# Kernel optimization log

Measured on AMD Instinct MI355X. Metric: run time of the kernel, lower is better.

The kernel has to match this reference:

```python
import jax, jax.numpy as jnp
import numpy as np

DIM = 320; HEADS = 8; DHEAD = 40; CTX_DIM = 768
INNER = HEADS * DHEAD; FF_INNER = 4 * DIM
B = 1; N = 4096; M = 77
SCALE = DHEAD ** -0.5


def setup_inputs() -> dict:
    key = jax.random.key(0)
    ks = jax.random.split(key, 16)
    p = lambda i, shape: jax.random.normal(ks[i], shape, dtype=jnp.float32) * 0.02
    return {
        "x": jax.random.normal(ks[0], (B, N, DIM), dtype=jnp.float32),
        "context": jax.random.normal(ks[1], (B, M, CTX_DIM), dtype=jnp.float32),
        "focused_attention_mask": jax.random.uniform(ks[2], (1, M, M), dtype=jnp.float32),
        "g1": jnp.ones((DIM,), jnp.float32), "b1": jnp.zeros((DIM,), jnp.float32),
        "g2": jnp.ones((DIM,), jnp.float32), "b2": jnp.zeros((DIM,), jnp.float32),
        "g3": jnp.ones((DIM,), jnp.float32), "b3": jnp.zeros((DIM,), jnp.float32),
        "Wq1": p(3, (DIM, INNER)), "Wk1": p(4, (DIM, INNER)), "Wv1": p(5, (DIM, INNER)),
        "Wo1": p(6, (INNER, DIM)), "bo1": jnp.zeros((DIM,), jnp.float32),
        "Wq2": p(7, (DIM, INNER)), "Wk2": p(8, (CTX_DIM, INNER)), "Wv2": p(9, (CTX_DIM, INNER)),
        "Wo2": p(10, (INNER, DIM)), "bo2": jnp.zeros((DIM,), jnp.float32),
        "Wff1": p(11, (DIM, 2 * FF_INNER)), "bff1": jnp.zeros((2 * FF_INNER,), jnp.float32),
        "Wff2": p(12, (FF_INNER, DIM)), "bff2": jnp.zeros((DIM,), jnp.float32),
        "use_fca": 1,
    }


def _ln(x, g, b):
    mu = x.mean(-1, keepdims=True)
    var = jnp.mean((x - mu) ** 2, -1, keepdims=True)
    return (x - mu) * jax.lax.rsqrt(var + 1e-5) * g + b


def _attn(xn, ctx, Wq, Wk, Wv, Wo, bo, fam, use_fca):
    b, n, _ = xn.shape
    heads = lambda t: t.reshape(b, t.shape[1], HEADS, DHEAD).transpose(0, 2, 1, 3)  # b h n d
    q, k, v = heads(xn @ Wq), heads(ctx @ Wk), heads(ctx @ Wv)
    sim = jnp.einsum('bhid,bhjd->bhij', q, k) * SCALE
    if use_fca:
        m = fam.shape[-1]  # fam: [1, m, m], batch must be 1 (repeat_interleave semantics)
        fw = jnp.einsum('bhqk,dk->bhqd', sim[..., :m], fam[0])
        fw = jnp.minimum(jnp.abs(fw), 1.0)
        fw = fw / (jnp.max(fw, axis=-1, keepdims=True) + 1e-6)
        fw = (fw > 0.6).astype(sim.dtype)
        sim = sim.at[..., :m].add((fw - 1.0) * 50.0)
    a = jax.nn.softmax(sim, axis=-1)
    o = jnp.einsum('bhij,bhjd->bhid', a, v).transpose(0, 2, 1, 3).reshape(b, n, INNER)
    return o @ Wo + bo


def reference(x, context, focused_attention_mask,
              g1, b1, g2, b2, g3, b3,
              Wq1, Wk1, Wv1, Wo1, bo1,
              Wq2, Wk2, Wv2, Wo2, bo2,
              Wff1, bff1, Wff2, bff2, use_fca):
    # attn1: self-attention (context=None in original -> use_fca forced to 0)
    h1 = _ln(x, g1, b1)
    x = _attn(h1, h1, Wq1, Wk1, Wv1, Wo1, bo1, None, 0) + x
    # attn2: cross-attention with focused-attention mask
    h2 = _ln(x, g2, b2)
    x = _attn(h2, context, Wq2, Wk2, Wv2, Wo2, bo2, focused_attention_mask, int(use_fca)) + x
    # GEGLU feed-forward
    h3 = _ln(x, g3, b3)
    proj = h3 @ Wff1 + bff1
    a_, gate = jnp.split(proj, 2, axis=-1)
    x = (a_ * jax.nn.gelu(gate, approximate=False)) @ Wff2 + bff2 + x
    return x
```

## Files before the change

kernel.cpp:

```cpp
#include <hip/hip_runtime.h>
#include <math.h>

typedef __bf16 bf16_t;
typedef __bf16 bf16x8 __attribute__((ext_vector_type(8)));
typedef __bf16 bf16x4 __attribute__((ext_vector_type(4)));
typedef float  f32x4  __attribute__((ext_vector_type(4)));
typedef _Float16 f16_t;
typedef _Float16 f16x4 __attribute__((ext_vector_type(4)));
typedef _Float16 f16x8 __attribute__((ext_vector_type(8)));
typedef __fp16 hf16x2 __attribute__((ext_vector_type(2)));

static constexpr float ATT_SCALE = 0.15811388300841897f;
static constexpr float SC2 = 0.22811031f;
static constexpr float LOG2E = 1.4426950408889634f;

__device__ __forceinline__ bf16_t f2b(float f) {
  unsigned u = __float_as_uint(f);
  u = (u + 0x7fffu + ((u >> 16) & 1u)) >> 16;
  unsigned short s = (unsigned short)u;
  bf16_t r;
  *(unsigned short*)&r = s;
  return r;
}
__device__ __forceinline__ float b2f(bf16_t b) {
  unsigned short s = *(const unsigned short*)&b;
  return __uint_as_float(((unsigned)s) << 16);
}
__device__ __forceinline__ void sto(float v, float* p)  { *p = v; }
__device__ __forceinline__ void sto(float v, bf16_t* p) { *p = f2b(v); }
__device__ __forceinline__ unsigned pkh2(float a, float b) {
  hf16x2 h = __builtin_amdgcn_cvt_pkrtz(a, b);
  return *(unsigned*)&h;
}

__global__ __launch_bounds__(256) void prep_ln_kernel(
    const float* __restrict__ Wq1, const float* __restrict__ Wk1, const float* __restrict__ Wv1,
    const float* __restrict__ Wo1, const float* __restrict__ Wq2,
    const float* __restrict__ Wk2, const float* __restrict__ Wv2, const float* __restrict__ Wo2,
    const float* __restrict__ Wff1, const float* __restrict__ Wff2,
    const float* __restrict__ fam,
    bf16_t* __restrict__ wqkvt, bf16_t* __restrict__ wo1t, float* __restrict__ wkv2t,
    bf16_t* __restrict__ wo2t, bf16_t* __restrict__ wff1t, bf16_t* __restrict__ wff2t,
    bf16_t* __restrict__ wq2th, bf16_t* __restrict__ wq2tl,
    bf16_t* __restrict__ famh, bf16_t* __restrict__ faml,
    bf16_t* __restrict__ zpad,
    const float* __restrict__ x, const float* __restrict__ g1, const float* __restrict__ b1,
    bf16_t* __restrict__ h1b)
{
  const int b = blockIdx.x;
  const int tid = threadIdx.x;

  if (b >= 634) {
    const int bb = b - 634;
    const int lane = tid & 63;
    const int row = bb * 4 + (tid >> 6);
    const float* xr = x + (size_t)row * 320;
    float v[5], s = 0.f, s2 = 0.f;
#pragma unroll
    for (int i = 0; i < 5; i++) { v[i] = xr[lane + i*64]; s += v[i]; s2 += v[i]*v[i]; }
#pragma unroll
    for (int o = 32; o; o >>= 1) { s += __shfl_xor(s, o); s2 += __shfl_xor(s2, o); }
    float mu = s * (1.f/320.f);
    float rs = rsqrtf(fmaxf(s2*(1.f/320.f) - mu*mu, 0.f) + 1e-5f);
#pragma unroll
    for (int i = 0; i < 5; i++) {
      int c = lane + i*64;
      h1b[(size_t)row*320 + c] = f2b((v[i]-mu)*rs*g1[c] + b1[c]);
    }
    return;
  }

  if (b >= 570) {
    for (int idx = (b - 570)*256 + tid; idx < 9216 + 135168; idx += 64*256) {
      if (idx < 9216) {
        int d = idx / 96, k = idx - d*96;
        float v = (d < 77 && k < 77) ? fam[d*77 + k] : 0.f;
        bf16_t h = f2b(v);
        famh[idx] = h;
        faml[idx] = f2b(v - b2f(h));
      } else {
        zpad[idx - 9216] = f2b(0.f);
      }
    }
    return;
  }

  __shared__ float T[64][65];
  const float* src; int S, O, n0, k0, mode;
  float scale = 1.f;
  bf16_t* outb = nullptr; float* outf = nullptr;
  int nadj;

  if (b < 75) {
    int tn = b / 5, tk = b - tn*5;
    n0 = tn*64; k0 = tk*64; S = 320; O = 320; mode = 0; outb = wqkvt;
    if (n0 < 320)      { src = Wq1; nadj = n0;       scale = SC2; }
    else if (n0 < 640) { src = Wk1; nadj = n0 - 320; }
    else               { src = Wv1; nadj = n0 - 640; }
  } else if (b < 100) {
    int b2 = b - 75; int tn = b2 / 5, tk = b2 - tn*5;
    n0 = tn*64; k0 = tk*64; S = 320; O = 320; mode = 0; outb = wo1t; src = Wo1; nadj = n0;
  } else if (b < 220) {
    int b2 = b - 100; int tn = b2 / 12, tk = b2 - tn*12;
    n0 = tn*64; k0 = tk*64; S = 320; O = 768; mode = 1; outf = wkv2t;
    if (n0 < 320) { src = Wk2; nadj = n0; } else { src = Wv2; nadj = n0 - 320; }
  } else if (b < 245) {
    int b2 = b - 220; int tn = b2 / 5, tk = b2 - tn*5;
    n0 = tn*64; k0 = tk*64; S = 320; O = 320; mode = 0; outb = wo2t; src = Wo2; nadj = n0;
  } else if (b < 445) {
    int b2 = b - 245; int tn = b2 / 5, tk = b2 - tn*5;
    n0 = tn*64; k0 = tk*64; S = 2560; O = 320; mode = 0; outb = wff1t; src = Wff1; nadj = n0;
  } else if (b < 545) {
    int b2 = b - 445; int tn = b2 / 20, tk = b2 - tn*20;
    n0 = tn*64; k0 = tk*64; S = 320; O = 1280; mode = 0; outb = wff2t; src = Wff2; nadj = n0;
  } else {
    int b2 = b - 545; int tn = b2 / 5, tk = b2 - tn*5;
    n0 = tn*64; k0 = tk*64; S = 320; O = 320; mode = 2; src = Wq2; nadj = n0;
  }

  const int r4 = tid >> 6;
  const int c  = tid & 63;
  const float* srcp = src + nadj;
#pragma unroll
  for (int i = 0; i < 16; i++) {
    int r = i*4 + r4;
    T[c][r] = srcp[(size_t)(k0 + r)*S + c] * scale;
  }
  __syncthreads();
#pragma unroll
  for (int i = 0; i < 16; i++) {
    int r = i*4 + r4;
    float v = T[r][c];
    size_t oi = (size_t)(n0 + r)*O + k0 + c;
    if (mode == 0) {
      outb[oi] = f2b(v);
    } else if (mode == 1) {
      outf[oi] = v;
    } else {
      bf16_t h = f2b(v);
      wq2th[oi] = h;
      wq2tl[oi] = f2b(v - b2f(h));
    }
  }
}

template<typename OT>
__global__ __launch_bounds__(256) void ln_kernel(
    const float* __restrict__ x, const float* __restrict__ g, const float* __restrict__ b,
    OT* __restrict__ out)
{
  const int lane = threadIdx.x & 63;
  const int row = blockIdx.x * 4 + (threadIdx.x >> 6);
  const float* xr = x + (size_t)row * 320;
  float v[5], s = 0.f, s2 = 0.f;
#pragma unroll
  for (int i = 0; i < 5; i++) { v[i] = xr[lane + i*64]; s += v[i]; s2 += v[i]*v[i]; }
#pragma unroll
  for (int o = 32; o; o >>= 1) { s += __shfl_xor(s, o); s2 += __shfl_xor(s2, o); }
  float mu = s * (1.f/320.f);
  float rs = rsqrtf(fmaxf(s2*(1.f/320.f) - mu*mu, 0.f) + 1e-5f);
#pragma unroll
  for (int i = 0; i < 5; i++) {
    int c = lane + i*64;
    sto((v[i]-mu)*rs*g[c] + b[c], &out[(size_t)row*320 + c]);
  }
}

__global__ __launch_bounds__(256) void ln2_split_kernel(
    const float* __restrict__ x, const float* __restrict__ g, const float* __restrict__ b,
    bf16_t* __restrict__ hi, bf16_t* __restrict__ lo)
{
  const int lane = threadIdx.x & 63;
  const int row = blockIdx.x * 4 + (threadIdx.x >> 6);
  const float* xr = x + (size_t)row * 320;
  float v[5], s = 0.f, s2 = 0.f;
#pragma unroll
  for (int i = 0; i < 5; i++) { v[i] = xr[lane + i*64]; s += v[i]; s2 += v[i]*v[i]; }
#pragma unroll
  for (int o = 32; o; o >>= 1) { s += __shfl_xor(s, o); s2 += __shfl_xor(s2, o); }
  float mu = s * (1.f/320.f);
  float rs = rsqrtf(fmaxf(s2*(1.f/320.f) - mu*mu, 0.f) + 1e-5f);
#pragma unroll
  for (int i = 0; i < 5; i++) {
    int c = lane + i*64;
    float y = (v[i]-mu)*rs*g[c] + b[c];
    bf16_t h = f2b(y);
    hi[(size_t)row*320 + c] = h;
    lo[(size_t)row*320 + c] = f2b(y - b2f(h));
  }
}

__global__ __launch_bounds__(256) void kv2_dot_kernel(
    const float* __restrict__ ctx, const float* __restrict__ wkv2t,
    bf16_t* __restrict__ k2h, bf16_t* __restrict__ k2l, bf16_t* __restrict__ v2t)
{
  __shared__ float4 Bs[16][193];
  const int tid = threadIdx.x;
  const int nb = blockIdx.x % 40, ms = blockIdx.x / 40;
  const int n0 = nb*16;
  for (int e = tid; e < 16*192; e += 256) {
    int row = e / 192, c4 = e - row*192;
    Bs[row][c4] = *(const float4*)(wkv2t + (size_t)(n0+row)*768 + c4*4);
  }
  __syncthreads();
  const int g = tid >> 4, q = tid & 15;
  const int mlo = ms*20;
  const int mhi = (mlo + 20 > 77) ? 77 : mlo + 20;
  for (int m = mlo; m < mhi; m++) {
    const float4* a = (const float4*)(ctx + (size_t)m*768);
    float acc = 0.f;
#pragma unroll
    for (int i = 0; i < 12; i++) {
      float4 av = a[i*16+q], bv = Bs[g][i*16+q];
      acc += av.x*bv.x + av.y*bv.y + av.z*bv.z + av.w*bv.w;
    }
#pragma unroll
    for (int o = 8; o; o >>= 1) acc += __shfl_xor(acc, o);
    if (q == 0) {
      int n = n0 + g;
      if (n < 320) {
        int h = n / 40, d = n - h*40;
        int idx = h*6144 + m*64 + d;
        bf16_t hh = f2b(acc);
        k2h[idx] = hh;
        k2l[idx] = f2b(acc - b2f(hh));
      } else {
        int n2 = n - 320; int h = n2 / 40, d = n2 - h*40;
        v2t[h*4608 + d*96 + m] = f2b(acc);
      }
    }
  }
}

__global__ __launch_bounds__(256) void repack_vt_kernel(
    const bf16_t* __restrict__ qkvb, f16_t* __restrict__ vpack, bf16_t* __restrict__ kpack)
{
  __shared__ f16_t T[64*44];
  const int tid = threadIdx.x;
  const int t0 = blockIdx.x * 64, h = blockIdx.y;
  for (int e = tid; e < 320; e += 256) {
    int t = e / 5, c8 = (e - t*5) * 8;
    bf16x8 v = *(const bf16x8*)(qkvb + (size_t)(t0+t)*960 + 640 + h*40 + c8);
    f16_t* dst = &T[t*44 + c8];
#pragma unroll
    for (int j = 0; j < 8; j++) dst[j] = (f16_t)b2f(v[j]);
  }
  __syncthreads();
  for (int e = tid; e < 3072; e += 256) {
    int dt = e >> 10;
    int r  = e & 1023;
    int g2 = r >> 9, o = r & 511;
    int lane = o >> 3, j = o & 7;
    int qd = lane >> 4, ln = lane & 15;
    int d = dt*16 + ln;
    int key = g2*32 + ((j & 4) ? 16 : 0) + qd*4 + (j & 3);
    float val;
    if (d < 40)       val = (float)T[key*44 + d];
    else if (d == 40) val = 1.0f;
    else              val = 0.0f;
    vpack[(((size_t)h*3 + dt)*128 + (t0 >> 5) + g2)*512 + o] = (f16_t)val;
  }
  for (int e = tid; e < 2560; e += 256) {
    int g = e / 640, o = e - g*640;
    int key = t0 + g*16;
    bf16_t val;
    if (o < 512) {
      int lane = o >> 3, j = o & 7;
      int qd = lane >> 4, ln = lane & 15;
      val = qkvb[(size_t)(key + ln)*960 + 320 + h*40 + qd*8 + j];
    } else {
      int o2 = o - 512; int ln = o2 >> 3, j = o2 & 7;
      val = qkvb[(size_t)(key + ln)*960 + 320 + h*40 + 32 + j];
    }
    kpack[((size_t)h*256 + (t0 >> 4) + g)*640 + o] = val;
  }
}

__global__ __launch_bounds__(512, 4) void flash_self_kernel(
    const bf16_t* __restrict__ qkvb, const bf16_t* __restrict__ kpack,
    const f16_t* __restrict__ vpack,
    bf16_t* __restrict__ o1a)
{
  __shared__ float Red[12288];
  const int tid = threadIdx.x;
  const int w = tid >> 6, lane = tid & 63;
  const int ln = lane & 15, qd = lane >> 4;
  const int qh = w >> 2, kh = w & 3;
  const int h = blockIdx.x & 7;
  const int q0 = (blockIdx.x >> 3) * 64;

  const int kgbase = h*256 + kh*2;
  const int vgbase = h*384 + kh;
  const int lko = lane*8;

  bf16x8 zero8 = {};
  bf16x8 bq[2][2];
#pragma unroll
  for (int nt = 0; nt < 2; nt++) {
    const bf16_t* qp = qkvb + (size_t)(q0 + qh*32 + nt*16 + ln)*960 + h*40;
    bq[nt][0] = *(const bf16x8*)(qp + qd*8);
    bq[nt][1] = (qd == 0) ? *(const bf16x8*)(qp + 32) : zero8;
  }

  f32x4 zero4 = {0.f,0.f,0.f,0.f};
  f32x4 oacc[3][2];
#pragma unroll
  for (int a = 0; a < 3; a++)
#pragma unroll
    for (int b = 0; b < 2; b++) oacc[a][b] = zero4;

#define FS_LOADK(DST, K0)                                                       \
  {                                                                             \
    const bf16_t* kp_ = kpack + ((size_t)kgbase + ((K0) >> 4)) * 640;           \
    DST[0][0] = *(const bf16x8*)(kp_ + lko);                                    \
    DST[0][1] = (qd == 0) ? *(const bf16x8*)(kp_ + 512 + ln*8) : zero8;         \
    DST[1][0] = *(const bf16x8*)(kp_ + 640 + lko);                              \
    DST[1][1] = (qd == 0) ? *(const bf16x8*)(kp_ + 1152 + ln*8) : zero8;        \
  }

#define FS_LOADV(DST, K0)                                                       \
  {                                                                             \
    _Pragma("unroll")                                                           \
    for (int dt_ = 0; dt_ < 3; dt_++)                                           \
      DST[dt_] = *(const f16x8*)(vpack + ((size_t)vgbase + dt_*128 + ((K0) >> 5)) * 512 + lko); \
  }

#define FS_COMPUTE(KA, VA)                                                      \
  {                                                                             \
    __builtin_amdgcn_s_setprio(1);                                              \
    _Pragma("unroll")                                                           \
    for (int nt = 0; nt < 2; nt++) {                                            \
      f32x4 s0 = __builtin_amdgcn_mfma_f32_16x16x32_bf16(KA[0][0], bq[nt][0], zero4, 0,0,0); \
      s0 = __builtin_amdgcn_mfma_f32_16x16x32_bf16(KA[0][1], bq[nt][1], s0, 0,0,0); \
      f32x4 s1 = __builtin_amdgcn_mfma_f32_16x16x32_bf16(KA[1][0], bq[nt][0], zero4, 0,0,0); \
      s1 = __builtin_amdgcn_mfma_f32_16x16x32_bf16(KA[1][1], bq[nt][1], s1, 0,0,0); \
      uint4 u_;                                                                 \
      u_.x = pkh2(__builtin_amdgcn_exp2f(s0[0]), __builtin_amdgcn_exp2f(s0[1])); \
      u_.y = pkh2(__builtin_amdgcn_exp2f(s0[2]), __builtin_amdgcn_exp2f(s0[3])); \
      u_.z = pkh2(__builtin_amdgcn_exp2f(s1[0]), __builtin_amdgcn_exp2f(s1[1])); \
      u_.w = pkh2(__builtin_amdgcn_exp2f(s1[2]), __builtin_amdgcn_exp2f(s1[3])); \
      f16x8 pb = *(f16x8*)&u_;                                                  \
      _Pragma("unroll")                                                         \
      for (int dt = 0; dt < 3; dt++)                                            \
        oacc[dt][nt] = __builtin_amdgcn_mfma_f32_16x16x32_f16(VA[dt], pb, oacc[dt][nt], 0,0,0); \
    }                                                                           \
    __builtin_amdgcn_s_setprio(0);                                              \
  }

  bf16x8 ka[2][2], kb[2][2];
  f16x8 va[3], vb[3];
  FS_LOADK(ka, 0);
  FS_LOADV(va, 0);
#pragma unroll 1
  for (int it = 0; it < 32; it += 2) {
    const int k0 = it*128;
    FS_LOADK(kb, k0 + 128);
    FS_LOADV(vb, k0 + 128);
    FS_COMPUTE(ka, va);
    FS_LOADK(ka, (it + 2 < 32) ? (k0 + 256) : 0);
    FS_LOADV(va, (it + 2 < 32) ? (k0 + 256) : 0);
    FS_COMPUTE(kb, vb);
  }
#undef FS_LOADK
#undef FS_LOADV
#undef FS_COMPUTE

#pragma unroll
  for (int nt = 0; nt < 2; nt++)
#pragma unroll
    for (int dt = 0; dt < 3; dt++)
      *(f32x4*)&Red[((w*2 + nt)*3 + dt)*256 + ln*16 + qd*4] = oacc[dt][nt];
  __syncthreads();
  const int dgrp = tid & 7, lq = (tid >> 3) & 15, ntw = (tid >> 7) & 1, qh2 = tid >> 8;
  float l = Red[(((qh2*4 + 0)*2 + ntw)*3 + 2)*256 + lq*16 + 8]
          + Red[(((qh2*4 + 1)*2 + ntw)*3 + 2)*256 + lq*16 + 8]
          + Red[(((qh2*4 + 2)*2 + ntw)*3 + 2)*256 + lq*16 + 8]
          + Red[(((qh2*4 + 3)*2 + ntw)*3 + 2)*256 + lq*16 + 8];
  float inv = 1.f / l;
  bf16_t* obase = o1a + (size_t)(q0 + qh2*32 + ntw*16 + lq)*320 + h*40;
#pragma unroll
  for (int i = 0; i < 5; i++) {
    int d = dgrp + i*8;
    int dt = d >> 4, dr = d & 15;
    float o = Red[(((qh2*4 + 0)*2 + ntw)*3 + dt)*256 + lq*16 + dr]
            + Red[(((qh2*4 + 1)*2 + ntw)*3 + dt)*256 + lq*16 + dr]
            + Red[(((qh2*4 + 2)*2 + ntw)*3 + dt)*256 + lq*16 + dr]
            + Red[(((qh2*4 + 3)*2 + ntw)*3 + dt)*256 + lq*16 + dr];
    obase[d] = f2b(o * inv);
  }
}

__global__ __launch_bounds__(256) void attn_cross_kernel(
    const float* __restrict__ q2, const bf16_t* __restrict__ k2h, const bf16_t* __restrict__ k2l,
    const bf16_t* __restrict__ famh, const bf16_t* __restrict__ faml,
    const bf16_t* __restrict__ v2t, const int* __restrict__ use_fca,
    bf16_t* __restrict__ o2)
{
  __shared__ bf16_t SMh[4][16*96];
  __shared__ bf16_t SMl[4][16*96];
  __shared__ bf16_t PAs[4][16*96];
  const int tid = threadIdx.x;
  const int w = tid >> 6, lane = tid & 63;
  const int ln = lane & 15, qd = lane >> 4;
  const int h = blockIdx.x & 7;
  const int q0 = (blockIdx.x >> 3)*64 + w*16;
  const int fca = use_fca[0];
  bf16_t* smh = SMh[w];
  bf16_t* sml = SMl[w];
  bf16_t* pa  = PAs[w];

  {
    bf16x4 z = {};
    int q = lane >> 2, c = 80 + (lane & 3)*4;
    *(bf16x4*)&smh[q*96 + c] = z;
    *(bf16x4*)&sml[q*96 + c] = z;
    *(bf16x4*)&pa [q*96 + c] = z;
  }

  bf16x8 zero8 = {};
  bf16x8 aqh0, aql0, aqh1 = zero8, aql1 = zero8;
  {
    const float* qp = q2 + (size_t)(q0 + ln)*320 + h*40;
    float4 v0 = *(const float4*)(qp + qd*8);
    float4 v1 = *(const float4*)(qp + qd*8 + 4);
    float qv[8] = {v0.x,v0.y,v0.z,v0.w,v1.x,v1.y,v1.z,v1.w};
#pragma unroll
    for (int i = 0; i < 8; i++) {
      bf16_t hh = f2b(qv[i]);
      aqh0[i] = hh; aql0[i] = f2b(qv[i] - b2f(hh));
    }
    if (qd == 0) {
      float4 u0 = *(const float4*)(qp + 32);
      float4 u1 = *(const float4*)(qp + 36);
      float uv[8] = {u0.x,u0.y,u0.z,u0.w,u1.x,u1.y,u1.z,u1.w};
#pragma unroll
      for (int i = 0; i < 8; i++) {
        bf16_t hh = f2b(uv[i]);
        aqh1[i] = hh; aql1[i] = f2b(uv[i] - b2f(hh));
      }
    }
  }

  f32x4 zero4 = {0.f,0.f,0.f,0.f};
  float ss[5][4];
  __builtin_amdgcn_s_setprio(1);
#pragma unroll
  for (int nt = 0; nt < 5; nt++) {
    const bf16_t* kb = k2h + ((size_t)h*96 + nt*16 + ln)*64 + qd*8;
    const bf16_t* kl = k2l + ((size_t)h*96 + nt*16 + ln)*64 + qd*8;
    bf16x8 kh0 = *(const bf16x8*)kb;
    bf16x8 kh1 = *(const bf16x8*)(kb + 32);
    bf16x8 kl0 = *(const bf16x8*)kl;
    bf16x8 kl1 = *(const bf16x8*)(kl + 32);
    f32x4 s;
    s = __builtin_amdgcn_mfma_f32_16x16x32_bf16(aqh0, kl0, zero4, 0, 0, 0);
    s = __builtin_amdgcn_mfma_f32_16x16x32_bf16(aql0, kh0, s, 0, 0, 0);
    s = __builtin_amdgcn_mfma_f32_16x16x32_bf16(aqh0, kh0, s, 0, 0, 0);
    s = __builtin_amdgcn_mfma_f32_16x16x32_bf16(aqh1, kl1, s, 0, 0, 0);
    s = __builtin_amdgcn_mfma_f32_16x16x32_bf16(aql1, kh1, s, 0, 0, 0);
    s = __builtin_amdgcn_mfma_f32_16x16x32_bf16(aqh1, kh1, s, 0, 0, 0);
#pragma unroll
    for (int r = 0; r < 4; r++) {
      float sv = s[r] * ATT_SCALE;
      ss[nt][r] = sv;
      bf16_t hh = f2b(sv);
      smh[(qd*4 + r)*96 + nt*16 + ln] = hh;
      sml[(qd*4 + r)*96 + nt*16 + ln] = f2b(sv - b2f(hh));
    }
  }
  __builtin_amdgcn_s_setprio(0);

  f32x4 facc[5];
#pragma unroll
  for (int nt = 0; nt < 5; nt++) facc[nt] = zero4;
  __builtin_amdgcn_s_setprio(1);
#pragma unroll
  for (int c = 0; c < 3; c++) {
    bf16x8 sah = *(const bf16x8*)&smh[ln*96 + c*32 + qd*8];
    bf16x8 sal = *(const bf16x8*)&sml[ln*96 + c*32 + qd*8];
#pragma unroll
    for (int nt = 0; nt < 5; nt++) {
      bf16x8 fh8 = *(const bf16x8*)(famh + ((size_t)(nt*16 + ln))*96 + c*32 + qd*8);
      bf16x8 fl8 = *(const bf16x8*)(faml + ((size_t)(nt*16 + ln))*96 + c*32 + qd*8);
      facc[nt] = __builtin_amdgcn_mfma_f32_16x16x32_bf16(sah, fl8, facc[nt], 0, 0, 0);
      facc[nt] = __builtin_amdgcn_mfma_f32_16x16x32_bf16(sal, fh8, facc[nt], 0, 0, 0);
      facc[nt] = __builtin_amdgcn_mfma_f32_16x16x32_bf16(sah, fh8, facc[nt], 0, 0, 0);
    }
  }
  __builtin_amdgcn_s_setprio(0);

  float pr[5][4];
  if (fca) {
    float fwv[5][4], fm[4];
#pragma unroll
    for (int nt = 0; nt < 5; nt++)
#pragma unroll
      for (int r = 0; r < 4; r++) fwv[nt][r] = fminf(fabsf(facc[nt][r]), 1.f);
#pragma unroll
    for (int r = 0; r < 4; r++) {
      float m = fmaxf(fmaxf(fwv[0][r], fwv[1][r]), fmaxf(fwv[2][r], fmaxf(fwv[3][r], fwv[4][r])));
#pragma unroll
      for (int o = 8; o; o >>= 1) m = fmaxf(m, __shfl_xor(m, o));
      fm[r] = m;
    }
#pragma unroll
    for (int nt = 0; nt < 5; nt++)
#pragma unroll
      for (int r = 0; r < 4; r++) {
        float lg = ss[nt][r] - ((fwv[nt][r] > 0.6f*(fm[r] + 1e-6f)) ? 0.f : 50.f);
        pr[nt][r] = __builtin_amdgcn_exp2f(lg * LOG2E);
      }
  } else {
#pragma unroll
    for (int nt = 0; nt < 5; nt++)
#pragma unroll
      for (int r = 0; r < 4; r++)
        pr[nt][r] = __builtin_amdgcn_exp2f(ss[nt][r] * LOG2E);
  }
  if (ln >= 13) {
#pragma unroll
    for (int r = 0; r < 4; r++) pr[4][r] = 0.f;
  }
  float l_[4] = {0.f,0.f,0.f,0.f};
#pragma unroll
  for (int nt = 0; nt < 5; nt++)
#pragma unroll
    for (int r = 0; r < 4; r++) {
      l_[r] += pr[nt][r];
      pa[(qd*4 + r)*96 + nt*16 + ln] = f2b(pr[nt][r]);
    }
#pragma unroll
  for (int r = 0; r < 4; r++)
#pragma unroll
    for (int o = 8; o; o >>= 1) l_[r] += __shfl_xor(l_[r], o);

  f32x4 oacc[3];
#pragma unroll
  for (int nt = 0; nt < 3; nt++) oacc[nt] = zero4;
  __builtin_amdgcn_s_setprio(1);
#pragma unroll
  for (int c = 0; c < 3; c++) {
    bf16x8 paf = *(const bf16x8*)&pa[ln*96 + c*32 + qd*8];
#pragma unroll
    for (int nt = 0; nt < 3; nt++) {
      bf16x8 vb = *(const bf16x8*)(v2t + ((size_t)h*48 + nt*16 + ln)*96 + c*32 + qd*8);
      oacc[nt] = __builtin_amdgcn_mfma_f32_16x16x32_bf16(paf, vb, oacc[nt], 0, 0, 0);
    }
  }
  __builtin_amdgcn_s_setprio(0);
  float inv[4];
#pragma unroll
  for (int r = 0; r < 4; r++) inv[r] = 1.f / l_[r];
#pragma unroll
  for (int nt = 0; nt < 3; nt++) {
    int d = nt*16 + ln;
    if (d < 40) {
#pragma unroll
      for (int r = 0; r < 4; r++)
        o2[(size_t)(q0 + qd*4 + r)*320 + h*40 + d] = f2b(oacc[nt][r]*inv[r]);
    }
  }
}

template<int OUT_BF16>
__global__ __launch_bounds__(256) void gemm_bf16_kernel(
    const bf16_t* __restrict__ A, const bf16_t* __restrict__ Bt,
    const float* __restrict__ bias, const float* __restrict__ resid,
    void* __restrict__ Cout, int M, int N, int K)
{
  __shared__ bf16_t As[128][72];
  __shared__ bf16_t Bs[64][72];
  const int tid = threadIdx.x;
  const int m0 = blockIdx.x * 128, n0 = blockIdx.y * 64;
  const int w = tid >> 6, lane = tid & 63;
  const int wr = w >> 1, wc = w & 1;
  const int ln = lane & 15, qd = lane >> 4;
  f32x4 zero = {0.f, 0.f, 0.f, 0.f};
  f32x4 acc[4][2];
#pragma unroll
  for (int a = 0; a < 4; a++)
#pragma unroll
    for (int b = 0; b < 2; b++) acc[a][b] = zero;

  for (int k0 = 0; k0 < K; k0 += 64) {
    __syncthreads();
#pragma unroll
    for (int i = 0; i < 4; i++) {
      int vid = tid + i*256;
      int r = vid >> 3, c8 = (vid & 7) * 8;
      *(bf16x8*)&As[r][c8] = *(const bf16x8*)(A + (size_t)(m0+r)*K + k0 + c8);
    }
#pragma unroll
    for (int i = 0; i < 2; i++) {
      int vid = tid + i*256;
      int r = vid >> 3, c8 = (vid & 7) * 8;
      *(bf16x8*)&Bs[r][c8] = *(const bf16x8*)(Bt + (size_t)(n0+r)*K + k0 + c8);
    }
    __syncthreads();
#pragma unroll
    for (int c = 0; c < 2; c++) {
      bf16x8 af[4], bfr[2];
#pragma unroll
      for (int mt = 0; mt < 4; mt++)
        af[mt] = *(const bf16x8*)&As[wr*64 + mt*16 + ln][c*32 + qd*8];
#pragma unroll
      for (int nt = 0; nt < 2; nt++)
        bfr[nt] = *(const bf16x8*)&Bs[wc*32 + nt*16 + ln][c*32 + qd*8];
#pragma unroll
      for (int mt = 0; mt < 4; mt++)
#pragma unroll
        for (int nt = 0; nt < 2; nt++)
          acc[mt][nt] = __builtin_amdgcn_mfma_f32_16x16x32_bf16(af[mt], bfr[nt], acc[mt][nt], 0, 0, 0);
    }
  }
#pragma unroll
  for (int mt = 0; mt < 4; mt++)
#pragma unroll
    for (int nt = 0; nt < 2; nt++)
#pragma unroll
      for (int r = 0; r < 4; r++) {
        int gm = m0 + wr*64 + mt*16 + qd*4 + r;
        int gn = n0 + wc*32 + nt*16 + ln;
        float v = acc[mt][nt][r];
        if (bias)  v += bias[gn];
        if (resid) v += resid[(size_t)gm*N + gn];
        if (OUT_BF16) sto(v, &((bf16_t*)Cout)[(size_t)gm*N + gn]);
        else          sto(v, &((float*)Cout)[(size_t)gm*N + gn]);
      }
}

template<int OUT_BF16>
__global__ __launch_bounds__(256) void gemm_bf16_32_kernel(
    const bf16_t* __restrict__ A, const bf16_t* __restrict__ Bt,
    const float* __restrict__ bias, const float* __restrict__ resid,
    void* __restrict__ Cout, int M, int N, int K)
{
  __shared__ bf16_t As[32][72];
  __shared__ bf16_t Bs[64][72];
  const int tid = threadIdx.x;
  const int m0 = blockIdx.x * 32, n0 = blockIdx.y * 64;
  const int w = tid >> 6, lane = tid & 63;
  const int wr = w >> 1, wc = w & 1;
  const int ln = lane & 15, qd = lane >> 4;
  f32x4 zero = {0.f, 0.f, 0.f, 0.f};
  f32x4 acc[2];
  acc[0] = zero; acc[1] = zero;

  for (int k0 = 0; k0 < K; k0 += 64) {
    __syncthreads();
    {
      int r = tid >> 3, c8 = (tid & 7) * 8;
      *(bf16x8*)&As[r][c8] = *(const bf16x8*)(A + (size_t)(m0+r)*K + k0 + c8);
    }
#pragma unroll
    for (int i = 0; i < 2; i++) {
      int vid = tid + i*256;
      int r = vid >> 3, c8 = (vid & 7) * 8;
      *(bf16x8*)&Bs[r][c8] = *(const bf16x8*)(Bt + (size_t)(n0+r)*K + k0 + c8);
    }
    __syncthreads();
#pragma unroll
    for (int c = 0; c < 2; c++) {
      bf16x8 af = *(const bf16x8*)&As[wr*16 + ln][c*32 + qd*8];
#pragma unroll
      for (int nt = 0; nt < 2; nt++) {
        bf16x8 bfr = *(const bf16x8*)&Bs[wc*32 + nt*16 + ln][c*32 + qd*8];
        acc[nt] = __builtin_amdgcn_mfma_f32_16x16x32_bf16(af, bfr, acc[nt], 0, 0, 0);
      }
    }
  }
#pragma unroll
  for (int nt = 0; nt < 2; nt++)
#pragma unroll
    for (int r = 0; r < 4; r++) {
      int gm = m0 + wr*16 + qd*4 + r;
      int gn = n0 + wc*32 + nt*16 + ln;
      float v = acc[nt][r];
      if (bias)  v += bias[gn];
      if (resid) v += resid[(size_t)gm*N + gn];
      if (OUT_BF16) sto(v, &((bf16_t*)Cout)[(size_t)gm*N + gn]);
      else          sto(v, &((float*)Cout)[(size_t)gm*N + gn]);
    }
}

__global__ __launch_bounds__(256) void gemm3_32_kernel(
    const bf16_t* __restrict__ Ah, const bf16_t* __restrict__ Al,
    const bf16_t* __restrict__ Bth, const bf16_t* __restrict__ Btl,
    float* __restrict__ C, int M, int N, int K)
{
  __shared__ bf16_t Ash[32][72];
  __shared__ bf16_t Asl[32][72];
  __shared__ bf16_t Bsh[64][72];
  __shared__ bf16_t Bsl[64][72];
  const int tid = threadIdx.x;
  const int m0 = blockIdx.x * 32, n0 = blockIdx.y * 64;
  const int w = tid >> 6, lane = tid & 63;
  const int wr = w >> 1, wc = w & 1;
  const int ln = lane & 15, qd = lane >> 4;
  f32x4 zero = {0.f, 0.f, 0.f, 0.f};
  f32x4 acc[2];
  acc[0] = zero; acc[1] = zero;

  for (int k0 = 0; k0 < K; k0 += 64) {
    __syncthreads();
    {
      int r = tid >> 3, c8 = (tid & 7) * 8;
      *(bf16x8*)&Ash[r][c8] = *(const bf16x8*)(Ah + (size_t)(m0+r)*K + k0 + c8);
      *(bf16x8*)&Asl[r][c8] = *(const bf16x8*)(Al + (size_t)(m0+r)*K + k0 + c8);
    }
#pragma unroll
    for (int i = 0; i < 2; i++) {
      int vid = tid + i*256;
      int r = vid >> 3, c8 = (vid & 7) * 8;
      *(bf16x8*)&Bsh[r][c8] = *(const bf16x8*)(Bth + (size_t)(n0+r)*K + k0 + c8);
      *(bf16x8*)&Bsl[r][c8] = *(const bf16x8*)(Btl + (size_t)(n0+r)*K + k0 + c8);
    }
    __syncthreads();
#pragma unroll
    for (int c = 0; c < 2; c++) {
      bf16x8 afh = *(const bf16x8*)&Ash[wr*16 + ln][c*32 + qd*8];
      bf16x8 afl = *(const bf16x8*)&Asl[wr*16 + ln][c*32 + qd*8];
#pragma unroll
      for (int nt = 0; nt < 2; nt++) {
        bf16x8 bfh = *(const bf16x8*)&Bsh[wc*32 + nt*16 + ln][c*32 + qd*8];
        bf16x8 bfl = *(const bf16x8*)&Bsl[wc*32 + nt*16 + ln][c*32 + qd*8];
        acc[nt] = __builtin_amdgcn_mfma_f32_16x16x32_bf16(afh, bfl, acc[nt], 0, 0, 0);
        acc[nt] = __builtin_amdgcn_mfma_f32_16x16x32_bf16(afl, bfh, acc[nt], 0, 0, 0);
        acc[nt] = __builtin_amdgcn_mfma_f32_16x16x32_bf16(afh, bfh, acc[nt], 0, 0, 0);
      }
    }
  }
#pragma unroll
  for (int nt = 0; nt < 2; nt++)
#pragma unroll
    for (int r = 0; r < 4; r++) {
      int gm = m0 + wr*16 + qd*4 + r;
      int gn = n0 + wc*32 + nt*16 + ln;
      C[(size_t)gm*N + gn] = acc[nt][r];
    }
}

__global__ __launch_bounds__(256) void gemm_geglu_kernel(
    const bf16_t* __restrict__ A, const bf16_t* __restrict__ Bt,
    const float* __restrict__ bias, bf16_t* __restrict__ gg, int K)
{
  __shared__ bf16_t As[128][72];
  __shared__ bf16_t Ba[64][72];
  __shared__ bf16_t Bg[64][72];
  const int tid = threadIdx.x;
  const int m0 = blockIdx.x * 128, n0 = blockIdx.y * 64;
  const int w = tid >> 6, lane = tid & 63;
  const int wr = w >> 1, wc = w & 1;
  const int ln = lane & 15, qd = lane >> 4;
  f32x4 zero = {0.f, 0.f, 0.f, 0.f};
  f32x4 acca[4][2], accg[4][2];
#pragma unroll
  for (int a = 0; a < 4; a++)
#pragma unroll
    for (int b = 0; b < 2; b++) { acca[a][b] = zero; accg[a][b] = zero; }

  for (int k0 = 0; k0 < K; k0 += 64) {
    __syncthreads();
#pragma unroll
    for (int i = 0; i < 4; i++) {
      int vid = tid + i*256;
      int r = vid >> 3, c8 = (vid & 7) * 8;
      *(bf16x8*)&As[r][c8] = *(const bf16x8*)(A + (size_t)(m0+r)*K + k0 + c8);
    }
#pragma unroll
    for (int i = 0; i < 2; i++) {
      int vid = tid + i*256;
      int r = vid >> 3, c8 = (vid & 7) * 8;
      *(bf16x8*)&Ba[r][c8] = *(const bf16x8*)(Bt + (size_t)(n0+r)*K + k0 + c8);
      *(bf16x8*)&Bg[r][c8] = *(const bf16x8*)(Bt + (size_t)(n0+r+1280)*K + k0 + c8);
    }
    __syncthreads();
#pragma unroll
    for (int c = 0; c < 2; c++) {
      bf16x8 af[4], ba[2], bg[2];
#pragma unroll
      for (int mt = 0; mt < 4; mt++)
        af[mt] = *(const bf16x8*)&As[wr*64 + mt*16 + ln][c*32 + qd*8];
#pragma unroll
      for (int nt = 0; nt < 2; nt++) {
        ba[nt] = *(const bf16x8*)&Ba[wc*32 + nt*16 + ln][c*32 + qd*8];
        bg[nt] = *(const bf16x8*)&Bg[wc*32 + nt*16 + ln][c*32 + qd*8];
      }
#pragma unroll
      for (int mt = 0; mt < 4; mt++)
#pragma unroll
        for (int nt = 0; nt < 2; nt++) {
          acca[mt][nt] = __builtin_amdgcn_mfma_f32_16x16x32_bf16(af[mt], ba[nt], acca[mt][nt], 0, 0, 0);
          accg[mt][nt] = __builtin_amdgcn_mfma_f32_16x16x32_bf16(af[mt], bg[nt], accg[mt][nt], 0, 0, 0);
        }
    }
  }
#pragma unroll
  for (int mt = 0; mt < 4; mt++)
#pragma unroll
    for (int nt = 0; nt < 2; nt++)
#pragma unroll
      for (int r = 0; r < 4; r++) {
        int gm = m0 + wr*64 + mt*16 + qd*4 + r;
        int gn = n0 + wc*32 + nt*16 + ln;
        float va = acca[mt][nt][r] + bias[gn];
        float vg = accg[mt][nt][r] + bias[1280 + gn];
        float ge = 0.5f * vg * (1.f + erff(vg * 0.70710678118654752f));
        gg[(size_t)gm*1280 + gn] = f2b(va * ge);
      }
}

extern "C" void kernel_launch(void* const* d_in, const int* in_sizes, int n_in,
                              void* d_out, int out_size, void* d_ws, size_t ws_size,
                              hipStream_t stream)
{
  const float* x    = (const float*)d_in[0];
  const float* ctx  = (const float*)d_in[1];
  const float* fam  = (const float*)d_in[2];
  const float* g1   = (const float*)d_in[3];
  const float* b1   = (const float*)d_in[4];
  const float* g2   = (const float*)d_in[5];
  const float* b2   = (const float*)d_in[6];
  const float* g3   = (const float*)d_in[7];
  const float* b3   = (const float*)d_in[8];
  const float* Wq1  = (const float*)d_in[9];
  const float* Wk1  = (const float*)d_in[10];
  const float* Wv1  = (const float*)d_in[11];
  const float* Wo1  = (const float*)d_in[12];
  const float* bo1  = (const float*)d_in[13];
  const float* Wq2  = (const float*)d_in[14];
  const float* Wk2  = (const float*)d_in[15];
  const float* Wv2  = (const float*)d_in[16];
  const float* Wo2  = (const float*)d_in[17];
  const float* bo2  = (const float*)d_in[18];
  const float* Wff1 = (const float*)d_in[19];
  const float* bff1 = (const float*)d_in[20];
  const float* Wff2 = (const float*)d_in[21];
  const float* bff2 = (const float*)d_in[22];
  const int*   ufca = (const int*)d_in[23];

  char* ws = (char*)d_ws;
  bf16_t* qkvb = (bf16_t*)(ws + 0);
  f16_t*  vpack = (f16_t*)(ws + 7864320);
  bf16_t* kpack = (bf16_t*)(ws + 11010048);
  bf16_t* h1b  = (bf16_t*)(ws + 13631488);
  bf16_t* h2hi = (bf16_t*)(ws + 16252928);
  bf16_t* h2lo = (bf16_t*)(ws + 18874368);
  float*  x2   = (float*)(ws + 21495808);
  float*  q2   = (float*)(ws + 26738688);
  bf16_t* o1a  = (bf16_t*)(ws + 26738688);
  bf16_t* o2   = (bf16_t*)(ws + 32178688);
  float*  x3   = (float*)(ws + 34800128);
  bf16_t* h3b  = (bf16_t*)(ws + 40043008);
  bf16_t* wqkvt = (bf16_t*)(ws + 42664448);
  bf16_t* wo1t  = (bf16_t*)(ws + 43278848);
  float*  wkv2t = (float*)(ws + 43483648);
  bf16_t* wo2t  = (bf16_t*)(ws + 45449728);
  bf16_t* wff1t = (bf16_t*)(ws + 45654528);
  bf16_t* wff2t = (bf16_t*)(ws + 47292928);
  bf16_t* wq2th = (bf16_t*)(ws + 48374272);
  bf16_t* wq2tl = (bf16_t*)(ws + 48579072);
  bf16_t* famh  = (bf16_t*)(ws + 48783872);
  bf16_t* faml  = (bf16_t*)(ws + 48802304);
  bf16_t* k2h   = (bf16_t*)(ws + 48820736);
  bf16_t* k2l   = (bf16_t*)(ws + 48919040);
  bf16_t* v2t   = (bf16_t*)(ws + 49017344);
  bf16_t* gg   = (bf16_t*)(ws + 21495808);

  float* xout = (float*)d_out;

  prep_ln_kernel<<<1658, 256, 0, stream>>>(Wq1, Wk1, Wv1, Wo1, Wq2, Wk2, Wv2, Wo2, Wff1, Wff2, fam,
                                           wqkvt, wo1t, wkv2t, wo2t, wff1t, wff2t, wq2th, wq2tl,
                                           famh, faml, k2h, x, g1, b1, h1b);
  gemm_bf16_kernel<1><<<dim3(32,15), 256, 0, stream>>>(h1b, wqkvt, nullptr, nullptr, qkvb, 4096, 960, 320);
  repack_vt_kernel<<<dim3(64,8), 256, 0, stream>>>(qkvb, vpack, kpack);
  flash_self_kernel<<<512, 512, 0, stream>>>(qkvb, kpack, vpack, o1a);
  gemm_bf16_32_kernel<0><<<dim3(128,5), 256, 0, stream>>>(o1a, wo1t, bo1, x, x2, 4096, 320, 320);
  ln2_split_kernel<<<1024, 256, 0, stream>>>(x2, g2, b2, h2hi, h2lo);
  gemm3_32_kernel<<<dim3(128,5), 256, 0, stream>>>(h2hi, h2lo, wq2th, wq2tl, q2, 4096, 320, 320);
  kv2_dot_kernel<<<160, 256, 0, stream>>>(ctx, wkv2t, k2h, k2l, v2t);
  attn_cross_kernel<<<512, 256, 0, stream>>>(q2, k2h, k2l, famh, faml, v2t, ufca, o2);
  gemm_bf16_32_kernel<0><<<dim3(128,5), 256, 0, stream>>>(o2, wo2t, bo2, x2, x3, 4096, 320, 320);
  ln_kernel<bf16_t><<<1024, 256, 0, stream>>>(x3, g3, b3, h3b);
  gemm_geglu_kernel<<<dim3(32,20), 256, 0, stream>>>(h3b, wff1t, bff1, gg, 320);
  gemm_bf16_32_kernel<0><<<dim3(128,5), 256, 0, stream>>>(gg, wff2t, bff2, x3, xout, 4096, 320, 1280);
}
```

Before: 258.2 us.

## Load GEMM tiles via direct global-to-LDS loads with XOR-swizzled layout

Replaces the register-staged global loads and LDS stores in the three bf16 GEMM kernels with global_load_lds 16-byte direct transfers into unpadded LDS tiles. The tiles are XOR-swizzled on 16-byte chunks, and the fragment reads use the matching swizzle, so bank conflicts are avoided without the previous padding. This cuts VGPR traffic and instruction count in the load phase. It relies on the 16-byte global_load_lds variant being supported on gfx950, and the swizzle indexing has to be exactly right for correctness.

```diff
diff --git a/kernel.cpp b/kernel.cpp
--- a/kernel.cpp
+++ b/kernel.cpp
@@ -31,6 +31,10 @@
 __device__ __forceinline__ unsigned pkh2(float a, float b) {
   hf16x2 h = __builtin_amdgcn_cvt_pkrtz(a, b);
   return *(unsigned*)&h;
+}
+__device__ __forceinline__ void gl_lds16(const void* g, void* l) {
+  __builtin_amdgcn_global_load_lds((const __attribute__((address_space(1))) unsigned*)g,
+                                   (__attribute__((address_space(3))) unsigned*)l, 16, 0, 0);
 }
 
 __global__ __launch_bounds__(256) void prep_ln_kernel(
@@ -568,13 +572,16 @@
     const float* __restrict__ bias, const float* __restrict__ resid,
     void* __restrict__ Cout, int M, int N, int K)
 {
-  __shared__ bf16_t As[128][72];
-  __shared__ bf16_t Bs[64][72];
+  __shared__ __align__(16) bf16_t As[128][64];
+  __shared__ __align__(16) bf16_t Bs[64][64];
   const int tid = threadIdx.x;
   const int m0 = blockIdx.x * 128, n0 = blockIdx.y * 64;
   const int w = tid >> 6, lane = tid & 63;
   const int wr = w >> 1, wc = w & 1;
   const int ln = lane & 15, qd = lane >> 4;
+  const int lr = lane >> 3, lsw = (lane & 7) ^ lr;
+  char* asb = (char*)&As[0][0];
+  char* bsb = (char*)&Bs[0][0];
   f32x4 zero = {0.f, 0.f, 0.f, 0.f};
   f32x4 acc[4][2];
 #pragma unroll
@@ -585,27 +592,22 @@
   for (int k0 = 0; k0 < K; k0 += 64) {
     __syncthreads();
 #pragma unroll
-    for (int i = 0; i < 4; i++) {
-      int vid = tid + i*256;
-      int r = vid >> 3, c8 = (vid & 7) * 8;
-      *(bf16x8*)&As[r][c8] = *(const bf16x8*)(A + (size_t)(m0+r)*K + k0 + c8);
-    }
-#pragma unroll
-    for (int i = 0; i < 2; i++) {
-      int vid = tid + i*256;
-      int r = vid >> 3, c8 = (vid & 7) * 8;
-      *(bf16x8*)&Bs[r][c8] = *(const bf16x8*)(Bt + (size_t)(n0+r)*K + k0 + c8);
-    }
+    for (int i = 0; i < 4; i++)
+      gl_lds16(A + (size_t)(m0 + (i*4 + w)*8 + lr)*K + k0 + lsw*8, asb + (i*4 + w)*1024);
+#pragma unroll
+    for (int i = 0; i < 2; i++)
+      gl_lds16(Bt + (size_t)(n0 + (i*4 + w)*8 + lr)*K + k0 + lsw*8, bsb + (i*4 + w)*1024);
     __syncthreads();
 #pragma unroll
     for (int c = 0; c < 2; c++) {
+      const int sa = (((c*4 + qd) ^ (ln & 7))) * 8;
       bf16x8 af[4], bfr[2];
 #pragma unroll
       for (int mt = 0; mt < 4; mt++)
-        af[mt] = *(const bf16x8*)&As[wr*64 + mt*16 + ln][c*32 + qd*8];
+        af[mt] = *(const bf16x8*)&As[wr*64 + mt*16 + ln][sa];
 #pragma unroll
       for (int nt = 0; nt < 2; nt++)
-        bfr[nt] = *(const bf16x8*)&Bs[wc*32 + nt*16 + ln][c*32 + qd*8];
+        bfr[nt] = *(const bf16x8*)&Bs[wc*32 + nt*16 + ln][sa];
 #pragma unroll
       for (int mt = 0; mt < 4; mt++)
 #pragma unroll
@@ -635,36 +637,34 @@
     const float* __restrict__ bias, const float* __restrict__ resid,
     void* __restrict__ Cout, int M, int N, int K)
 {
-  __shared__ bf16_t As[32][72];
-  __shared__ bf16_t Bs[64][72];
+  __shared__ __align__(16) bf16_t As[32][64];
+  __shared__ __align__(16) bf16_t Bs[64][64];
   const int tid = threadIdx.x;
   const int m0 = blockIdx.x * 32, n0 = blockIdx.y * 64;
   const int w = tid >> 6, lane = tid & 63;
   const int wr = w >> 1, wc = w & 1;
   const int ln = lane & 15, qd = lane >> 4;
+  const int lr = lane >> 3, lsw = (lane & 7) ^ lr;
+  char* asb = (char*)&As[0][0];
+  char* bsb = (char*)&Bs[0][0];
   f32x4 zero = {0.f, 0.f, 0.f, 0.f};
   f32x4 acc[2];
   acc[0] = zero; acc[1] = zero;
 
   for (int k0 = 0; k0 < K; k0 += 64) {
     __syncthreads();
-    {
-      int r = tid >> 3, c8 = (tid & 7) * 8;
-      *(bf16x8*)&As[r][c8] = *(const bf16x8*)(A + (size_t)(m0+r)*K + k0 + c8);
-    }
-#pragma unroll
-    for (int i = 0; i < 2; i++) {
-      int vid = tid + i*256;
-      int r = vid >> 3, c8 = (vid & 7) * 8;
-      *(bf16x8*)&Bs[r][c8] = *(const bf16x8*)(Bt + (size_t)(n0+r)*K + k0 + c8);
-    }
+    gl_lds16(A + (size_t)(m0 + w*8 + lr)*K + k0 + lsw*8, asb + w*1024);
+#pragma unroll
+    for (int i = 0; i < 2; i++)
+      gl_lds16(Bt + (size_t)(n0 + (i*4 + w)*8 + lr)*K + k0 + lsw*8, bsb + (i*4 + w)*1024);
     __syncthreads();
 #pragma unroll
     for (int c = 0; c < 2; c++) {
-      bf16x8 af = *(const bf16x8*)&As[wr*16 + ln][c*32 + qd*8];
+      const int sa = (((c*4 + qd) ^ (ln & 7))) * 8;
+      bf16x8 af = *(const bf16x8*)&As[wr*16 + ln][sa];
 #pragma unroll
       for (int nt = 0; nt < 2; nt++) {
-        bf16x8 bfr = *(const bf16x8*)&Bs[wc*32 + nt*16 + ln][c*32 + qd*8];
+        bf16x8 bfr = *(const bf16x8*)&Bs[wc*32 + nt*16 + ln][sa];
         acc[nt] = __builtin_amdgcn_mfma_f32_16x16x32_bf16(af, bfr, acc[nt], 0, 0, 0);
       }
     }
@@ -744,14 +744,18 @@
     const bf16_t* __restrict__ A, const bf16_t* __restrict__ Bt,
     const float* __restrict__ bias, bf16_t* __restrict__ gg, int K)
 {
-  __shared__ bf16_t As[128][72];
-  __shared__ bf16_t Ba[64][72];
-  __shared__ bf16_t Bg[64][72];
+  __shared__ __align__(16) bf16_t As[128][64];
+  __shared__ __align__(16) bf16_t Ba[64][64];
+  __shared__ __align__(16) bf16_t Bg[64][64];
   const int tid = threadIdx.x;
   const int m0 = blockIdx.x * 128, n0 = blockIdx.y * 64;
   const int w = tid >> 6, lane = tid & 63;
   const int wr = w >> 1, wc = w & 1;
   const int ln = lane & 15, qd = lane >> 4;
+  const int lr = lane >> 3, lsw = (lane & 7) ^ lr;
+  char* asb = (char*)&As[0][0];
+  char* bab = (char*)&Ba[0][0];
+  char* bgb = (char*)&Bg[0][0];
   f32x4 zero = {0.f, 0.f, 0.f, 0.f};
   f32x4 acca[4][2], accg[4][2];
 #pragma unroll
@@ -762,29 +766,25 @@
   for (int k0 = 0; k0 < K; k0 += 64) {
     __syncthreads();
 #pragma unroll
-    for (int i = 0; i < 4; i++) {
-      int vid = tid + i*256;
-      int r = vid >> 3, c8 = (vid & 7) * 8;
-      *(bf16x8*)&As[r][c8] = *(const bf16x8*)(A + (size_t)(m0+r)*K + k0 + c8);
-    }
+    for (int i = 0; i < 4; i++)
+      gl_lds16(A + (size_t)(m0 + (i*4 + w)*8 + lr)*K + k0 + lsw*8, asb + (i*4 + w)*1024);
 #pragma unroll
     for (int i = 0; i < 2; i++) {
-      int vid = tid + i*256;
-      int r = vid >> 3, c8 = (vid & 7) * 8;
-      *(bf16x8*)&Ba[r][c8] = *(const bf16x8*)(Bt + (size_t)(n0+r)*K + k0 + c8);
-      *(bf16x8*)&Bg[r][c8] = *(const bf16x8*)(Bt + (size_t)(n0+r+1280)*K + k0 + c8);
+      gl_lds16(Bt + (size_t)(n0 + (i*4 + w)*8 + lr)*K + k0 + lsw*8, bab + (i*4 + w)*1024);
+      gl_lds16(Bt + (size_t)(n0 + 1280 + (i*4 + w)*8 + lr)*K + k0 + lsw*8, bgb + (i*4 + w)*1024);
     }
     __syncthreads();
 #pragma unroll
     for (int c = 0; c < 2; c++) {
+      const int sa = (((c*4 + qd) ^ (ln & 7))) * 8;
       bf16x8 af[4], ba[2], bg[2];
 #pragma unroll
       for (int mt = 0; mt < 4; mt++)
-        af[mt] = *(const bf16x8*)&As[wr*64 + mt*16 + ln][c*32 + qd*8];
+        af[mt] = *(const bf16x8*)&As[wr*64 + mt*16 + ln][sa];
 #pragma unroll
       for (int nt = 0; nt < 2; nt++) {
-        ba[nt] = *(const bf16x8*)&Ba[wc*32 + nt*16 + ln][c*32 + qd*8];
-        bg[nt] = *(const bf16x8*)&Bg[wc*32 + nt*16 + ln][c*32 + qd*8];
+        ba[nt] = *(const bf16x8*)&Ba[wc*32 + nt*16 + ln][sa];
+        bg[nt] = *(const bf16x8*)&Bg[wc*32 + nt*16 + ln][sa];
       }
 #pragma unroll
       for (int mt = 0; mt < 4; mt++)
```

Result: no change. 254.3 us (-1.5%).
